# Optimization experiments

Measured on AMD Instinct MI355X. Metric: run time of the kernel, lower is better.

Reference implementation:

```python
import jax, jax.numpy as jnp
import numpy as np


def setup_inputs() -> dict:
    key = jax.random.key(0)
    ks = jax.random.split(key, 12)
    B, T, D, H = 64, 512, 256, 1024
    s = 0.01
    return {
        "x": jax.random.normal(ks[0], (B, T, D), jnp.float32),
        "Wd": jax.random.normal(ks[1], (D, H), jnp.float32) * s,
        "bd": jax.random.normal(ks[2], (H,), jnp.float32) * s,
        "Wz": jax.random.normal(ks[3], (D, H), jnp.float32) * s,
        "Wr": jax.random.normal(ks[4], (D, H), jnp.float32) * s,
        "Wh": jax.random.normal(ks[5], (D, H), jnp.float32) * s,
        "Uz": jax.random.normal(ks[6], (H, H), jnp.float32) * s,
        "Ur": jax.random.normal(ks[7], (H, H), jnp.float32) * s,
        "Uh": jax.random.normal(ks[8], (H, H), jnp.float32) * s,
        "bz": jax.random.normal(ks[9], (H,), jnp.float32) * s,
        "br": jax.random.normal(ks[10], (H,), jnp.float32) * s,
        "bh": jax.random.normal(ks[11], (H,), jnp.float32) * s,
    }


def reference(x, Wd, bd, Wz, Wr, Wh, Uz, Ur, Uh, bz, br, bh):
    # x: [B, T, D]. GRU-D recurrence with exponential decay of hidden state.
    B, T, D = x.shape
    H = Wd.shape[1]
    # Precompute all input projections in one batched GEMM each: [B, T, H]
    decay_in = jnp.einsum('btd,dh->bth', x, Wd) + bd
    xz = jnp.einsum('btd,dh->bth', x, Wz) + bz
    xr = jnp.einsum('btd,dh->bth', x, Wr) + br
    xh = jnp.einsum('btd,dh->bth', x, Wh) + bh
    gamma = jnp.exp(-jax.nn.relu(decay_in))  # decay factor per step

    def step(h_tm1, inputs):
        g_t, xz_t, xr_t, xh_t = inputs  # each [B, H]
        h_dec = g_t * h_tm1
        z_t = jax.nn.sigmoid(xz_t + h_dec @ Uz)
        r_t = jax.nn.sigmoid(xr_t + h_dec @ Ur)
        h_prop = jnp.tanh(xh_t + (r_t * h_dec) @ Uh)
        h_t = (1.0 - z_t) * h_dec + z_t * h_prop
        return h_t, h_t

    h0 = jnp.zeros((B, H), x.dtype)
    # scan over time: move T to leading axis
    seq = (jnp.swapaxes(gamma, 0, 1), jnp.swapaxes(xz, 0, 1),
           jnp.swapaxes(xr, 0, 1), jnp.swapaxes(xh, 0, 1))
    _, hs = jax.lax.scan(step, h0, seq)  # hs: [T, B, H]
    return jnp.swapaxes(hs, 0, 1)  # [B, T, H]
```

## Files before the change

### kernel.cpp

```cpp
#include <hip/hip_runtime.h>
#include <cstdint>
#include <cstddef>


#define NB 64
#define NT 512
#define ND 256
#define NH 1024

typedef _Float16 h2_t __attribute__((ext_vector_type(2)));
typedef _Float16 half8 __attribute__((ext_vector_type(8)));
typedef float f32x4 __attribute__((ext_vector_type(4)));
typedef uint32_t u32x4 __attribute__((ext_vector_type(4)));

__device__ __forceinline__ float fdot2(uint32_t a, uint32_t b, float acc) {
  h2_t ha = __builtin_bit_cast(h2_t, a);
  h2_t hb = __builtin_bit_cast(h2_t, b);
#if __has_builtin(__builtin_amdgcn_fdot2)
  return __builtin_amdgcn_fdot2(ha, hb, acc, false);
#else
  return acc + (float)ha[0] * (float)hb[0] + (float)ha[1] * (float)hb[1];
#endif
}

__device__ __forceinline__ uint32_t pack2(float a, float b) {
  h2_t v; v[0] = (_Float16)a; v[1] = (_Float16)b;
  return __builtin_bit_cast(uint32_t, v);
}
__device__ __forceinline__ uint16_t f2h(float x) {
  _Float16 v = (_Float16)x; return __builtin_bit_cast(uint16_t, v);
}
__device__ __forceinline__ float h2f(uint16_t u) {
  return (float)__builtin_bit_cast(_Float16, u);
}
__device__ __forceinline__ float sigm(float x) {
  return 1.f / (1.f + __expf(-x));
}
__device__ __forceinline__ float fast_tanh(float x) {
  float e = __expf(2.f * x);
  return 1.f - 2.f / (e + 1.f);
}
__device__ __forceinline__ float ldnt_h(const uint16_t* p) {
  return h2f(__builtin_nontemporal_load(p));
}
__device__ __forceinline__ void stnt_f(float* p, float v) {
  __builtin_nontemporal_store(v, p);
}

__device__ __forceinline__ u32x4 ld_cg_b128(const uint32_t* p) {
  u32x4 v;
  asm volatile("global_load_dwordx4 %0, %1, off sc0 sc1" : "=v"(v) : "v"(p) : "memory");
  return v;
}
__device__ __forceinline__ void st_cg_b128(uint32_t* p, u32x4 v) {
  asm volatile("global_store_dwordx4 %0, %1, off sc0 sc1" :: "v"(p), "v"(v) : "memory");
}
__device__ __forceinline__ void st_cg_b32(uint32_t* p, unsigned v) {
  asm volatile("global_store_dword %0, %1, off sc0 sc1" :: "v"(p), "v"(v) : "memory");
}
__device__ __forceinline__ unsigned ld_cg_b32w(const uint32_t* p) {
  unsigned v;
  asm volatile("global_load_dword %0, %1, off sc0 sc1\n\ts_waitcnt vmcnt(0)"
               : "=v"(v) : "v"(p) : "memory");
  return v;
}


__global__ void pack_x_k(const float2* __restrict__ x, uint32_t* __restrict__ x2, int n) {
  int stride = gridDim.x * blockDim.x;
  for (int i = blockIdx.x * blockDim.x + threadIdx.x; i < n; i += stride) {
    float2 v = x[i];
    x2[i] = pack2(v.x, v.y);
  }
}

__global__ void pack_rows_k(const float* __restrict__ src, uint32_t* __restrict__ dst, int K) {
  int n = (K >> 1) * NH;
  int stride = gridDim.x * blockDim.x;
  for (int i = blockIdx.x * blockDim.x + threadIdx.x; i < n; i += stride) {
    int kp = i >> 10, j = i & 1023;
    dst[i] = pack2(src[(2 * kp) * NH + j], src[(2 * kp + 1) * NH + j]);
  }
}

__global__ __launch_bounds__(256) void transpose_f2h_k(
    const float* __restrict__ src, uint16_t* __restrict__ dst) {
  __shared__ uint16_t lt[64][68];
  int tr = blockIdx.x & 15, tc = blockIdx.x >> 4;
  int tid = threadIdx.x;
  int r0 = tid >> 6, cc = tid & 63;
#pragma unroll
  for (int it = 0; it < 16; ++it) {
    int r = it * 4 + r0;
    lt[cc][r] = f2h(src[(size_t)(tr * 64 + r) * 1024 + tc * 64 + cc]);
  }
  __syncthreads();
#pragma unroll
  for (int it = 0; it < 16; ++it) {
    int c = it * 4 + r0;
    dst[(size_t)(tc * 64 + c) * 1024 + tr * 64 + cc] = lt[c][cc];
  }
}

__global__ __launch_bounds__(256) void proj_k(
    const uint32_t* __restrict__ x2, const uint32_t* __restrict__ W2,
    const float* __restrict__ bd, const float* __restrict__ bz,
    const float* __restrict__ br, const float* __restrict__ bh,
    uint16_t* __restrict__ g_gamma, uint16_t* __restrict__ g_xz,
    uint16_t* __restrict__ g_xr, uint16_t* __restrict__ g_xh) {
  __shared__ uint32_t xs[64 * 132];
  int wg = blockIdx.x;
  int rg = wg >> 6;
  int cg = wg & 63;
  int tid = threadIdx.x;

  const uint4* xsrc = (const uint4*)x2 + (size_t)rg * 64 * 32;
#pragma unroll
  for (int w = 0; w < 8; ++w) {
    int f = tid + w * 256;
    int row = f >> 5, q = f & 31;
    *(uint4*)&xs[row * 132 + q * 4] = xsrc[row * 32 + q];
  }
  __syncthreads();

  int a = cg >> 4;
  int j0 = (cg & 15) * 64 + (tid & 15) * 4;
  int tr = tid >> 4;
  const uint32_t* W2a = W2 + (size_t)a * (128 * 1024) + j0;

  float acc[4][4] = {};
#pragma unroll 4
  for (int kp = 0; kp < 128; ++kp) {
    uint32_t xv0 = xs[(tr * 4 + 0) * 132 + kp];
    uint32_t xv1 = xs[(tr * 4 + 1) * 132 + kp];
    uint32_t xv2 = xs[(tr * 4 + 2) * 132 + kp];
    uint32_t xv3 = xs[(tr * 4 + 3) * 132 + kp];
    uint4 wv = *(const uint4*)(W2a + (size_t)kp * 1024);
    acc[0][0] = fdot2(xv0, wv.x, acc[0][0]); acc[0][1] = fdot2(xv0, wv.y, acc[0][1]);
    acc[0][2] = fdot2(xv0, wv.z, acc[0][2]); acc[0][3] = fdot2(xv0, wv.w, acc[0][3]);
    acc[1][0] = fdot2(xv1, wv.x, acc[1][0]); acc[1][1] = fdot2(xv1, wv.y, acc[1][1]);
    acc[1][2] = fdot2(xv1, wv.z, acc[1][2]); acc[1][3] = fdot2(xv1, wv.w, acc[1][3]);
    acc[2][0] = fdot2(xv2, wv.x, acc[2][0]); acc[2][1] = fdot2(xv2, wv.y, acc[2][1]);
    acc[2][2] = fdot2(xv2, wv.z, acc[2][2]); acc[2][3] = fdot2(xv2, wv.w, acc[2][3]);
    acc[3][0] = fdot2(xv3, wv.x, acc[3][0]); acc[3][1] = fdot2(xv3, wv.y, acc[3][1]);
    acc[3][2] = fdot2(xv3, wv.z, acc[3][2]); acc[3][3] = fdot2(xv3, wv.w, acc[3][3]);
  }

  const float* bias = a == 0 ? bd : a == 1 ? bz : a == 2 ? br : bh;
  uint16_t* dst = a == 0 ? g_gamma : a == 1 ? g_xz : a == 2 ? g_xr : g_xh;
  float b0 = bias[j0], b1 = bias[j0 + 1], b2 = bias[j0 + 2], b3 = bias[j0 + 3];
#pragma unroll
  for (int i = 0; i < 4; ++i) {
    int n = rg * 64 + tr * 4 + i;
    int b = n >> 9, t = n & 511;
    float p0 = acc[i][0] + b0, p1 = acc[i][1] + b1;
    float p2 = acc[i][2] + b2, p3 = acc[i][3] + b3;
    if (a == 0) {
      p0 = __expf(-fmaxf(p0, 0.f)); p1 = __expf(-fmaxf(p1, 0.f));
      p2 = __expf(-fmaxf(p2, 0.f)); p3 = __expf(-fmaxf(p3, 0.f));
    }
    uint32_t* o = (uint32_t*)(dst + (((size_t)(t * 64 + b)) << 10) + j0);
    o[0] = pack2(p0, p1);
    o[1] = pack2(p2, p3);
  }
}


__global__ __launch_bounds__(256, 1) void scan_k(
    const uint16_t* __restrict__ UzT, const uint16_t* __restrict__ UrT,
    const uint16_t* __restrict__ UhT,
    const uint16_t* __restrict__ g_gamma, const uint16_t* __restrict__ g_xz,
    const uint16_t* __restrict__ g_xr, const uint16_t* __restrict__ g_xh,
    uint16_t* __restrict__ Hdat, uint16_t* __restrict__ RHdat,
    uint32_t* __restrict__ Htag, uint32_t* __restrict__ RHtag,
    float* __restrict__ out) {
  __shared__ __align__(16) uint16_t Hp[9][1032];
  __shared__ __align__(16) uint16_t RHp[9][1032];
  __shared__ float red[4][4][256];
  __shared__ __align__(16) uint16_t pub16[8][32];

  const int tid = threadIdx.x;
  const int g = blockIdx.x & 7;
  const int slot = blockIdx.x >> 3;
  const int c0 = slot * 32;
  const int lane = tid & 63, w = tid >> 6;
  const int r16 = lane & 15, q = lane >> 4;

  for (int i = tid; i < 1032; i += 256) { Hp[8][i] = 0; RHp[8][i] = 0; }

  half8 Bz[2][8], Br[2][8], Bh[2][8];
#pragma unroll
  for (int ct = 0; ct < 2; ++ct) {
    const size_t colb = (size_t)(c0 + ct * 16 + r16) * 1024 + w * 256 + q * 8;
#pragma unroll
    for (int kc = 0; kc < 8; ++kc) {
      Bz[ct][kc] = *(const half8*)(UzT + colb + kc * 32);
      Br[ct][kc] = *(const half8*)(UrT + colb + kc * 32);
      Bh[ct][kc] = *(const half8*)(UhT + colb + kc * 32);
    }
  }
  __syncthreads();

  const uint16_t* aprow = Hp[r16 < 8 ? r16 : 8];
  const uint16_t* aprow2 = RHp[r16 < 8 ? r16 : 8];
  const int aoff = w * 256 + q * 8;

  const int ect = w & 1;
  const int ecol = c0 + ect * 16 + r16;
  const int erow = q * 4;

  uint32_t* mytagH = Htag + (g * 32 + slot) * 16;
  uint32_t* mytagR = RHtag + (g * 32 + slot) * 16;
  const uint32_t* tagH = Htag + (g * 32 + (tid & 31)) * 16;
  const uint32_t* tagR = RHtag + (g * 32 + (tid & 31)) * 16;

  auto poll_tags = [&](const uint32_t* tp, unsigned exp) {
    for (;;) {
      unsigned v = ld_cg_b32w(tp);
      __builtin_amdgcn_sched_barrier(0);
      if (__all((int)(v == exp))) break;
      __builtin_amdgcn_s_sleep(2);
    }
  };
  auto fill = [&](const uint16_t* dat, uint16_t (&panel)[9][1032]) {
    const uint32_t* src = (const uint32_t*)(dat +
        ((size_t)(g * 8 + (tid >> 5)) << 10) + (size_t)(tid & 31) * 32);
    u32x4 v0 = ld_cg_b128(src);
    u32x4 v1 = ld_cg_b128(src + 4);
    u32x4 v2 = ld_cg_b128(src + 8);
    u32x4 v3 = ld_cg_b128(src + 12);
    asm volatile("s_waitcnt vmcnt(0)" ::: "memory");
    __builtin_amdgcn_sched_barrier(0);
    uint16_t* dst = &panel[tid >> 5][(tid & 31) * 32];
    *(u32x4*)(dst + 0)  = v0;
    *(u32x4*)(dst + 8)  = v1;
    *(u32x4*)(dst + 16) = v2;
    *(u32x4*)(dst + 24) = v3;
  };
  auto publish = [&](uint16_t* dat, uint32_t* tagp, unsigned tagval) {
    if (tid < 32) {
      int r = tid >> 2;
      int cq = (tid & 3) * 8;
      uint32_t* dp = (uint32_t*)(dat + ((size_t)(g * 8 + r) << 10) + c0 + cq);
      st_cg_b128(dp, *(u32x4*)&pub16[r][cq]);
      asm volatile("s_waitcnt vmcnt(0)" ::: "memory");
      if (tid == 0) st_cg_b32(tagp, tagval);
    }
  };

  for (int t = 0; t < NT; ++t) {
    float xzv[4], xrv[4], xhv[4], gmv[4];
    {
      const int tg = (t + 1 < NT) ? t + 1 : t;
#pragma unroll
      for (int j = 0; j < 4; ++j) {
        int rr = erow + j; if (rr > 7) rr = 7;
        size_t base = (((size_t)(t * 64 + g * 8 + rr)) << 10) + ecol;
        if (w < 2) {
          xzv[j] = ldnt_h(&g_xz[base]);
          xhv[j] = ldnt_h(&g_xh[base]);
          gmv[j] = ldnt_h(&g_gamma[(((size_t)(tg * 64 + g * 8 + rr)) << 10) + ecol]);
          xrv[j] = 0.f;
        } else {
          xrv[j] = ldnt_h(&g_xr[base]);
          xzv[j] = xhv[j] = gmv[j] = 0.f;
        }
      }
    }

    poll_tags(tagH, (unsigned)t);
    fill(Hdat, Hp);
    __syncthreads();

    f32x4 az0 = {0.f,0.f,0.f,0.f}, az1 = {0.f,0.f,0.f,0.f};
    f32x4 ar0 = {0.f,0.f,0.f,0.f}, ar1 = {0.f,0.f,0.f,0.f};
#pragma unroll
    for (int kc = 0; kc < 8; ++kc) {
      half8 av = *(const half8*)(aprow + aoff + kc * 32);
      az0 = __builtin_amdgcn_mfma_f32_16x16x32_f16(av, Bz[0][kc], az0, 0, 0, 0);
      az1 = __builtin_amdgcn_mfma_f32_16x16x32_f16(av, Bz[1][kc], az1, 0, 0, 0);
      ar0 = __builtin_amdgcn_mfma_f32_16x16x32_f16(av, Br[0][kc], ar0, 0, 0, 0);
      ar1 = __builtin_amdgcn_mfma_f32_16x16x32_f16(av, Br[1][kc], ar1, 0, 0, 0);
    }
    *(f32x4*)&red[w][0][lane * 4] = az0;
    *(f32x4*)&red[w][1][lane * 4] = az1;
    *(f32x4*)&red[w][2][lane * 4] = ar0;
    *(f32x4*)&red[w][3][lane * 4] = ar1;
    __syncthreads();

    float zk[4] = {0.f,0.f,0.f,0.f}, hdk[4] = {0.f,0.f,0.f,0.f};
    {
      f32x4 s = *(const f32x4*)&red[0][w][lane * 4];
      s += *(const f32x4*)&red[1][w][lane * 4];
      s += *(const f32x4*)&red[2][w][lane * 4];
      s += *(const f32x4*)&red[3][w][lane * 4];
      if (lane < 32) {
        if (w < 2) {
#pragma unroll
          for (int j = 0; j < 4; ++j) {
            zk[j] = sigm(xzv[j] + s[j]);
            hdk[j] = h2f(Hp[erow + j][ecol]);
          }
        } else {
#pragma unroll
          for (int j = 0; j < 4; ++j) {
            float rg = sigm(xrv[j] + s[j]);
            float hd = h2f(Hp[erow + j][ecol]);
            pub16[erow + j][ect * 16 + r16] = f2h(rg * hd);
          }
        }
      }
    }
    __syncthreads();
    publish(RHdat, mytagR, (unsigned)(t + 1));

    poll_tags(tagR, (unsigned)(t + 1));
    fill(RHdat, RHp);
    __syncthreads();

    f32x4 ah0 = {0.f,0.f,0.f,0.f}, ah1 = {0.f,0.f,0.f,0.f};
#pragma unroll
    for (int kc = 0; kc < 8; ++kc) {
      half8 av = *(const half8*)(aprow2 + aoff + kc * 32);
      ah0 = __builtin_amdgcn_mfma_f32_16x16x32_f16(av, Bh[0][kc], ah0, 0, 0, 0);
      ah1 = __builtin_amdgcn_mfma_f32_16x16x32_f16(av, Bh[1][kc], ah1, 0, 0, 0);
    }
    *(f32x4*)&red[w][0][lane * 4] = ah0;
    *(f32x4*)&red[w][1][lane * 4] = ah1;
    __syncthreads();

    if (w < 2) {
      f32x4 s = *(const f32x4*)&red[0][w][lane * 4];
      s += *(const f32x4*)&red[1][w][lane * 4];
      s += *(const f32x4*)&red[2][w][lane * 4];
      s += *(const f32x4*)&red[3][w][lane * 4];
      if (lane < 32) {
#pragma unroll
        for (int j = 0; j < 4; ++j) {
          float hp = fast_tanh(xhv[j] + s[j]);
          float h = (1.f - zk[j]) * hdk[j] + zk[j] * hp;
          int b = g * 8 + erow + j;
          stnt_f(&out[((size_t)b * NT + t) * NH + ecol], h);
          pub16[erow + j][ect * 16 + r16] = f2h(gmv[j] * h);
        }
      }
    }
    __syncthreads();
    if (t + 1 < NT) publish(Hdat, mytagH, (unsigned)(t + 1));
  }
}


extern "C" void kernel_launch(void* const* d_in, const int* in_sizes, int n_in,
                              void* d_out, int out_size, void* d_ws, size_t ws_size,
                              hipStream_t stream) {
  const float* x  = (const float*)d_in[0];
  const float* Wd = (const float*)d_in[1];
  const float* bd = (const float*)d_in[2];
  const float* Wz = (const float*)d_in[3];
  const float* Wr = (const float*)d_in[4];
  const float* Wh = (const float*)d_in[5];
  const float* Uz = (const float*)d_in[6];
  const float* Ur = (const float*)d_in[7];
  const float* Uh = (const float*)d_in[8];
  const float* bz = (const float*)d_in[9];
  const float* br = (const float*)d_in[10];
  const float* bh = (const float*)d_in[11];
  float* out = (float*)d_out;

  char* ws = (char*)d_ws;
  size_t off = 0;
  auto take = [&](size_t bytes) -> char* {
    char* p = ws + off;
    off = (off + bytes + 255) & ~(size_t)255;
    return p;
  };
  uint32_t* x2  = (uint32_t*)take((size_t)32768 * 128 * 4);
  uint32_t* W2  = (uint32_t*)take((size_t)4 * 128 * 1024 * 4);
  uint16_t* UzT = (uint16_t*)take((size_t)1024 * 1024 * 2);
  uint16_t* UrT = (uint16_t*)take((size_t)1024 * 1024 * 2);
  uint16_t* UhT = (uint16_t*)take((size_t)1024 * 1024 * 2);
  uint16_t* g_gamma = (uint16_t*)take((size_t)NT * NB * NH * 2);
  uint16_t* g_xz   = (uint16_t*)take((size_t)NT * NB * NH * 2);
  uint16_t* g_xr   = (uint16_t*)take((size_t)NT * NB * NH * 2);
  uint16_t* g_xh   = (uint16_t*)take((size_t)NT * NB * NH * 2);
  uint16_t* Hdat   = (uint16_t*)take((size_t)NB * NH * 2);
  uint16_t* RHdat  = (uint16_t*)take((size_t)NB * NH * 2);
  uint32_t* Htag   = (uint32_t*)take((size_t)8 * 32 * 16 * 4);
  uint32_t* RHtag  = (uint32_t*)take((size_t)8 * 32 * 16 * 4);
  (void)ws_size; (void)in_sizes; (void)n_in; (void)out_size;

  (void)hipMemsetAsync(Hdat, 0, (size_t)NB * NH * 2, stream);
  (void)hipMemsetAsync(Htag, 0, (size_t)8 * 32 * 16 * 4, stream);
  (void)hipMemsetAsync(RHtag, 0, (size_t)8 * 32 * 16 * 4, stream);

  pack_x_k<<<2048, 256, 0, stream>>>((const float2*)x, x2, 32768 * 128);
  pack_rows_k<<<512, 256, 0, stream>>>(Wd, W2 + 0 * (128 * 1024), ND);
  pack_rows_k<<<512, 256, 0, stream>>>(Wz, W2 + 1 * (128 * 1024), ND);
  pack_rows_k<<<512, 256, 0, stream>>>(Wr, W2 + 2 * (128 * 1024), ND);
  pack_rows_k<<<512, 256, 0, stream>>>(Wh, W2 + 3 * (128 * 1024), ND);
  transpose_f2h_k<<<256, 256, 0, stream>>>(Uz, UzT);
  transpose_f2h_k<<<256, 256, 0, stream>>>(Ur, UrT);
  transpose_f2h_k<<<256, 256, 0, stream>>>(Uh, UhT);

  proj_k<<<32768, 256, 0, stream>>>(x2, W2, bd, bz, br, bh,
                                    g_gamma, g_xz, g_xr, g_xh);

  scan_k<<<256, 256, 0, stream>>>(UzT, UrT, UhT, g_gamma, g_xz, g_xr, g_xh,
                                  Hdat, RHdat, Htag, RHtag, out);
}
```

Measured before the change: 3.702 ms.

## Use MFMA for input projection and fuse x fp16 packing into it

Replaces the fdot2-based projection GEMM with MFMA 16x16x32 f16 instructions reading transposed fp16 weights. The input x is converted to fp16 directly while being loaded into shared memory, which removes the separate pack_x kernel and its intermediate buffer. The per-weight pack kernels become a generic transpose kernel. The projection may be a modest share of the total next to the sequential scan, and the new epilogue writes scattered 16-bit stores.

Result: no change. 3.721 ms (+0.5%).

```diff
diff --git a/kernel.cpp b/kernel.cpp
--- a/kernel.cpp
+++ b/kernel.cpp
@@ -12,16 +12,6 @@
 typedef _Float16 half8 __attribute__((ext_vector_type(8)));
 typedef float f32x4 __attribute__((ext_vector_type(4)));
 typedef uint32_t u32x4 __attribute__((ext_vector_type(4)));
-
-__device__ __forceinline__ float fdot2(uint32_t a, uint32_t b, float acc) {
-  h2_t ha = __builtin_bit_cast(h2_t, a);
-  h2_t hb = __builtin_bit_cast(h2_t, b);
-#if __has_builtin(__builtin_amdgcn_fdot2)
-  return __builtin_amdgcn_fdot2(ha, hb, acc, false);
-#else
-  return acc + (float)ha[0] * (float)hb[0] + (float)ha[1] * (float)hb[1];
-#endif
-}
 
 __device__ __forceinline__ uint32_t pack2(float a, float b) {
   h2_t v; v[0] = (_Float16)a; v[1] = (_Float16)b;
@@ -65,103 +55,78 @@
   return v;
 }
 
-
-__global__ void pack_x_k(const float2* __restrict__ x, uint32_t* __restrict__ x2, int n) {
-  int stride = gridDim.x * blockDim.x;
-  for (int i = blockIdx.x * blockDim.x + threadIdx.x; i < n; i += stride) {
-    float2 v = x[i];
-    x2[i] = pack2(v.x, v.y);
-  }
-}
-
-__global__ void pack_rows_k(const float* __restrict__ src, uint32_t* __restrict__ dst, int K) {
-  int n = (K >> 1) * NH;
-  int stride = gridDim.x * blockDim.x;
-  for (int i = blockIdx.x * blockDim.x + threadIdx.x; i < n; i += stride) {
-    int kp = i >> 10, j = i & 1023;
-    dst[i] = pack2(src[(2 * kp) * NH + j], src[(2 * kp + 1) * NH + j]);
-  }
-}
-
-__global__ __launch_bounds__(256) void transpose_f2h_k(
-    const float* __restrict__ src, uint16_t* __restrict__ dst) {
+__global__ __launch_bounds__(256) void transpose_f2h_g(
+    const float* __restrict__ src, uint16_t* __restrict__ dst, int R, int C) {
   __shared__ uint16_t lt[64][68];
-  int tr = blockIdx.x & 15, tc = blockIdx.x >> 4;
+  int tpc = C >> 6;
+  int tr = blockIdx.x / tpc, tc = blockIdx.x % tpc;
   int tid = threadIdx.x;
   int r0 = tid >> 6, cc = tid & 63;
 #pragma unroll
   for (int it = 0; it < 16; ++it) {
     int r = it * 4 + r0;
-    lt[cc][r] = f2h(src[(size_t)(tr * 64 + r) * 1024 + tc * 64 + cc]);
+    lt[cc][r] = f2h(src[(size_t)(tr * 64 + r) * C + tc * 64 + cc]);
   }
   __syncthreads();
 #pragma unroll
   for (int it = 0; it < 16; ++it) {
     int c = it * 4 + r0;
-    dst[(size_t)(tc * 64 + c) * 1024 + tr * 64 + cc] = lt[c][cc];
-  }
-}
-
-__global__ __launch_bounds__(256) void proj_k(
-    const uint32_t* __restrict__ x2, const uint32_t* __restrict__ W2,
+    dst[(size_t)(tc * 64 + c) * R + tr * 64 + cc] = lt[c][cc];
+  }
+}
+
+__global__ __launch_bounds__(256) void proj_mfma_k(
+    const float* __restrict__ x, const uint16_t* __restrict__ WT,
     const float* __restrict__ bd, const float* __restrict__ bz,
     const float* __restrict__ br, const float* __restrict__ bh,
     uint16_t* __restrict__ g_gamma, uint16_t* __restrict__ g_xz,
     uint16_t* __restrict__ g_xr, uint16_t* __restrict__ g_xh) {
-  __shared__ uint32_t xs[64 * 132];
-  int wg = blockIdx.x;
-  int rg = wg >> 6;
-  int cg = wg & 63;
-  int tid = threadIdx.x;
-
-  const uint4* xsrc = (const uint4*)x2 + (size_t)rg * 64 * 32;
-#pragma unroll
-  for (int w = 0; w < 8; ++w) {
-    int f = tid + w * 256;
-    int row = f >> 5, q = f & 31;
-    *(uint4*)&xs[row * 132 + q * 4] = xsrc[row * 32 + q];
+  __shared__ __align__(16) uint16_t As[64][264];
+  const int tid = threadIdx.x;
+  const int rg = blockIdx.x >> 6;
+  const int cg = blockIdx.x & 63;
+  const int lane = tid & 63, w = tid >> 6;
+  const int r16 = lane & 15, q = lane >> 4;
+
+#pragma unroll
+  for (int it = 0; it < 16; ++it) {
+    int idx = tid + it * 256;
+    int row = idx >> 6, c4 = (idx & 63) << 2;
+    float4 v = *(const float4*)(x + (size_t)(rg * 64 + row) * 256 + c4);
+    uint32_t* dp = (uint32_t*)&As[row][c4];
+    dp[0] = pack2(v.x, v.y);
+    dp[1] = pack2(v.z, v.w);
   }
   __syncthreads();
 
-  int a = cg >> 4;
-  int j0 = (cg & 15) * 64 + (tid & 15) * 4;
-  int tr = tid >> 4;
-  const uint32_t* W2a = W2 + (size_t)a * (128 * 1024) + j0;
-
-  float acc[4][4] = {};
-#pragma unroll 4
-  for (int kp = 0; kp < 128; ++kp) {
-    uint32_t xv0 = xs[(tr * 4 + 0) * 132 + kp];
-    uint32_t xv1 = xs[(tr * 4 + 1) * 132 + kp];
-    uint32_t xv2 = xs[(tr * 4 + 2) * 132 + kp];
-    uint32_t xv3 = xs[(tr * 4 + 3) * 132 + kp];
-    uint4 wv = *(const uint4*)(W2a + (size_t)kp * 1024);
-    acc[0][0] = fdot2(xv0, wv.x, acc[0][0]); acc[0][1] = fdot2(xv0, wv.y, acc[0][1]);
-    acc[0][2] = fdot2(xv0, wv.z, acc[0][2]); acc[0][3] = fdot2(xv0, wv.w, acc[0][3]);
-    acc[1][0] = fdot2(xv1, wv.x, acc[1][0]); acc[1][1] = fdot2(xv1, wv.y, acc[1][1]);
-    acc[1][2] = fdot2(xv1, wv.z, acc[1][2]); acc[1][3] = fdot2(xv1, wv.w, acc[1][3]);
-    acc[2][0] = fdot2(xv2, wv.x, acc[2][0]); acc[2][1] = fdot2(xv2, wv.y, acc[2][1]);
-    acc[2][2] = fdot2(xv2, wv.z, acc[2][2]); acc[2][3] = fdot2(xv2, wv.w, acc[2][3]);
-    acc[3][0] = fdot2(xv3, wv.x, acc[3][0]); acc[3][1] = fdot2(xv3, wv.y, acc[3][1]);
-    acc[3][2] = fdot2(xv3, wv.z, acc[3][2]); acc[3][3] = fdot2(xv3, wv.w, acc[3][3]);
-  }
-
+  const int a = cg >> 4;
+  const int cbase = (cg & 15) * 64;
+  const uint16_t* WTa = WT + (size_t)a * (1024 * 256);
   const float* bias = a == 0 ? bd : a == 1 ? bz : a == 2 ? br : bh;
   uint16_t* dst = a == 0 ? g_gamma : a == 1 ? g_xz : a == 2 ? g_xr : g_xh;
-  float b0 = bias[j0], b1 = bias[j0 + 1], b2 = bias[j0 + 2], b3 = bias[j0 + 3];
-#pragma unroll
-  for (int i = 0; i < 4; ++i) {
-    int n = rg * 64 + tr * 4 + i;
-    int b = n >> 9, t = n & 511;
-    float p0 = acc[i][0] + b0, p1 = acc[i][1] + b1;
-    float p2 = acc[i][2] + b2, p3 = acc[i][3] + b3;
-    if (a == 0) {
-      p0 = __expf(-fmaxf(p0, 0.f)); p1 = __expf(-fmaxf(p1, 0.f));
-      p2 = __expf(-fmaxf(p2, 0.f)); p3 = __expf(-fmaxf(p3, 0.f));
-    }
-    uint32_t* o = (uint32_t*)(dst + (((size_t)(t * 64 + b)) << 10) + j0);
-    o[0] = pack2(p0, p1);
-    o[1] = pack2(p2, p3);
+  const bool isg = (a == 0);
+
+  const uint16_t* arow = &As[w * 16 + r16][q * 8];
+
+#pragma unroll
+  for (int nt = 0; nt < 4; ++nt) {
+    int colg = cbase + nt * 16 + r16;
+    const uint16_t* bcol = WTa + (size_t)colg * 256 + q * 8;
+    f32x4 acc = {0.f, 0.f, 0.f, 0.f};
+#pragma unroll
+    for (int kc = 0; kc < 8; ++kc)
+      acc = __builtin_amdgcn_mfma_f32_16x16x32_f16(
+          *(const half8*)(arow + kc * 32), *(const half8*)(bcol + kc * 32),
+          acc, 0, 0, 0);
+    float bv = bias[colg];
+#pragma unroll
+    for (int j = 0; j < 4; ++j) {
+      int n = rg * 64 + w * 16 + q * 4 + j;
+      int b = n >> 9, t = n & 511;
+      float p = acc[j] + bv;
+      if (isg) p = __expf(-fmaxf(p, 0.f));
+      dst[(((size_t)(t * 64 + b)) << 10) + colg] = f2h(p);
+    }
   }
 }
 
@@ -375,8 +340,7 @@
     off = (off + bytes + 255) & ~(size_t)255;
     return p;
   };
-  uint32_t* x2  = (uint32_t*)take((size_t)32768 * 128 * 4);
-  uint32_t* W2  = (uint32_t*)take((size_t)4 * 128 * 1024 * 4);
+  uint16_t* WT  = (uint16_t*)take((size_t)4 * 1024 * 256 * 2);
   uint16_t* UzT = (uint16_t*)take((size_t)1024 * 1024 * 2);
   uint16_t* UrT = (uint16_t*)take((size_t)1024 * 1024 * 2);
   uint16_t* UhT = (uint16_t*)take((size_t)1024 * 1024 * 2);
@@ -394,17 +358,16 @@
   (void)hipMemsetAsync(Htag, 0, (size_t)8 * 32 * 16 * 4, stream);
   (void)hipMemsetAsync(RHtag, 0, (size_t)8 * 32 * 16 * 4, stream);
 
-  pack_x_k<<<2048, 256, 0, stream>>>((const float2*)x, x2, 32768 * 128);
-  pack_rows_k<<<512, 256, 0, stream>>>(Wd, W2 + 0 * (128 * 1024), ND);
-  pack_rows_k<<<512, 256, 0, stream>>>(Wz, W2 + 1 * (128 * 1024), ND);
-  pack_rows_k<<<512, 256, 0, stream>>>(Wr, W2 + 2 * (128 * 1024), ND);
-  pack_rows_k<<<512, 256, 0, stream>>>(Wh, W2 + 3 * (128 * 1024), ND);
-  transpose_f2h_k<<<256, 256, 0, stream>>>(Uz, UzT);
-  transpose_f2h_k<<<256, 256, 0, stream>>>(Ur, UrT);
-  transpose_f2h_k<<<256, 256, 0, stream>>>(Uh, UhT);
-
-  proj_k<<<32768, 256, 0, stream>>>(x2, W2, bd, bz, br, bh,
-                                    g_gamma, g_xz, g_xr, g_xh);
+  transpose_f2h_g<<<64, 256, 0, stream>>>(Wd, WT + 0 * (1024 * 256), 256, 1024);
+  transpose_f2h_g<<<64, 256, 0, stream>>>(Wz, WT + 1 * (1024 * 256), 256, 1024);
+  transpose_f2h_g<<<64, 256, 0, stream>>>(Wr, WT + 2 * (1024 * 256), 256, 1024);
+  transpose_f2h_g<<<64, 256, 0, stream>>>(Wh, WT + 3 * (1024 * 256), 256, 1024);
+  transpose_f2h_g<<<256, 256, 0, stream>>>(Uz, UzT, 1024, 1024);
+  transpose_f2h_g<<<256, 256, 0, stream>>>(Ur, UrT, 1024, 1024);
+  transpose_f2h_g<<<256, 256, 0, stream>>>(Uh, UhT, 1024, 1024);
+
+  proj_mfma_k<<<512 * 64, 256, 0, stream>>>(x, WT, bd, bz, br, bh,
+                                            g_gamma, g_xz, g_xr, g_xh);
 
   scan_k<<<256, 256, 0, stream>>>(UzT, UrT, UhT, g_gamma, g_xz, g_xr, g_xh,
                                   Hdat, RHdat, Htag, RHtag, out);
```
